# Kernel tuning notes

Hardware: AMD Instinct MI355X
Metric: run time of the kernel (lower is better)

## Reference

```python
import jax, jax.numpy as jnp
import numpy as np

NUM_TYPES = 4
EPS = 1e-5
NEG_SLOPE = 0.01  # nn.LeakyReLU default


def hetero_linear(x, node_type, W, b):
    # x: [N, Cin], W: [T, Cin, Cout], b: [T, Cout]
    # Grouped GEMM via type-masked batched matmul (T is small and fixed).
    onehot = jax.nn.one_hot(node_type, NUM_TYPES, dtype=x.dtype)  # [N, T]
    xt = onehot.T[:, :, None] * x[None, :, :]                      # [T, N, Cin]
    y = jnp.einsum('tni,tio->no', xt, W)                           # [N, Cout]
    return y + b[node_type]


def hetero_batchnorm(x, node_type, gamma, beta):
    # Per-type batch statistics over the nodes of each type (training-mode BN).
    ones = jnp.ones((x.shape[0],), dtype=x.dtype)
    cnt = jax.ops.segment_sum(ones, node_type, num_segments=NUM_TYPES)      # [T]
    cnt = jnp.maximum(cnt, 1.0)
    s = jax.ops.segment_sum(x, node_type, num_segments=NUM_TYPES)           # [T, C]
    ss = jax.ops.segment_sum(x * x, node_type, num_segments=NUM_TYPES)      # [T, C]
    mean = s / cnt[:, None]
    var = ss / cnt[:, None] - mean * mean  # biased variance, as BN uses
    xn = (x - mean[node_type]) * jax.lax.rsqrt(var[node_type] + EPS)
    return xn * gamma[node_type] + beta[node_type]


def setup_inputs() -> dict:
    key = jax.random.key(0)
    ks = jax.random.split(key, 12)
    N, CIN, H, COUT, T = 32768, 256, 512, 256, NUM_TYPES
    x = jax.random.normal(ks[0], (N, CIN), dtype=jnp.float32)
    node_type = jax.random.randint(ks[1], (N,), 0, T, dtype=jnp.int32)
    def lin(k, ci, co):
        k1, k2 = jax.random.split(k)
        scale = 1.0 / np.sqrt(ci)
        W = jax.random.uniform(k1, (T, ci, co), jnp.float32, -scale, scale)
        b = jax.random.uniform(k2, (T, co), jnp.float32, -scale, scale)
        return W, b
    W1, b1 = lin(ks[2], CIN, H)
    W2, b2 = lin(ks[3], H, H)
    W3, b3 = lin(ks[4], H, COUT)
    gamma1 = jnp.ones((T, H), jnp.float32)
    beta1 = jnp.zeros((T, H), jnp.float32)
    gamma2 = jnp.ones((T, H), jnp.float32)
    beta2 = jnp.zeros((T, H), jnp.float32)
    return {"x": x, "node_type": node_type,
            "W1": W1, "b1": b1, "W2": W2, "b2": b2, "W3": W3, "b3": b3,
            "gamma1": gamma1, "beta1": beta1, "gamma2": gamma2, "beta2": beta2}


def reference(x, node_type, W1, b1, W2, b2, W3, b3, gamma1, beta1, gamma2, beta2):
    # Layer 1: HeteroLinear -> HeteroBatchNorm -> LeakyReLU (dropout p=0 -> identity)
    h = hetero_linear(x, node_type, W1, b1)
    h = hetero_batchnorm(h, node_type, gamma1, beta1)
    h = jax.nn.leaky_relu(h, NEG_SLOPE)
    # Layer 2
    h = hetero_linear(h, node_type, W2, b2)
    h = hetero_batchnorm(h, node_type, gamma2, beta2)
    h = jax.nn.leaky_relu(h, NEG_SLOPE)
    # Layer 3: plain_last -> no norm/act
    out = hetero_linear(h, node_type, W3, b3)
    return out
```

## Files before the change

### kernel.cpp

```cpp
#include <hip/hip_runtime.h>
#include <cstdint>
#include <cstddef>

#define N_NODES 32768
#define CIN 256
#define HDIM 512
#define COUT_F 256
#define NTYPE 4
#define ALIGN_SEG 128
#define NPAD (N_NODES + NTYPE * ALIGN_SEG)
#define NROWBLK (NPAD / 128)
#define BN_EPS 1e-5f
#define SLOPE 0.01f

typedef unsigned short u16;
typedef __attribute__((ext_vector_type(8))) short bf16x8;
typedef __attribute__((ext_vector_type(4))) float f32x4;
typedef __attribute__((ext_vector_type(4))) u16 u16x4;

#define GLOBAL_AS __attribute__((address_space(1)))
#define LDS_AS __attribute__((address_space(3)))

__device__ __forceinline__ u16 f2bf(float f) {
  union { float f; unsigned u; } v{f};
  unsigned r = (v.u + 0x7FFF + ((v.u >> 16) & 1)) >> 16;
  return (u16)r;
}
__device__ __forceinline__ float bf2f(u16 b) {
  union { unsigned u; float f; } v;
  v.u = ((unsigned)b) << 16;
  return v.f;
}


__global__ void hist_kernel(const int* __restrict__ nt, int* __restrict__ blockHist) {
  __shared__ int h[NTYPE];
  int tid = threadIdx.x;
  if (tid < NTYPE) h[tid] = 0;
  __syncthreads();
  int i = blockIdx.x * 256 + tid;
  atomicAdd(&h[nt[i]], 1);
  __syncthreads();
  if (tid < NTYPE) blockHist[blockIdx.x * NTYPE + tid] = h[tid];
}

__global__ void scan_kernel(const int* __restrict__ blockHist, int* __restrict__ blockBase,
                            int* __restrict__ meta) {
  int tid = threadIdx.x;
  if (tid < NTYPE) {
    int run = 0;
    for (int b = 0; b < 128; ++b) {
      blockBase[b * NTYPE + tid] = run;
      run += blockHist[b * NTYPE + tid];
    }
    meta[tid] = run;
  }
  __syncthreads();
  if (tid == 0) {
    int s = 0;
    for (int t = 0; t < NTYPE; ++t) {
      meta[4 + t] = s;
      s += (meta[t] + ALIGN_SEG - 1) & ~(ALIGN_SEG - 1);
    }
    meta[8] = s;
  }
}

__global__ void rank_scatter_kernel(const int* __restrict__ nt, const int* __restrict__ blockBase,
                                    const int* __restrict__ meta, int* __restrict__ perm) {
  __shared__ int st[256];
  int tid = threadIdx.x;
  int i = blockIdx.x * 256 + tid;
  int t = nt[i];
  st[tid] = t;
  __syncthreads();
  int rank = 0;
  for (int j = 0; j < tid; ++j) rank += (st[j] == t) ? 1 : 0;
  perm[meta[4 + t] + blockBase[blockIdx.x * NTYPE + t] + rank] = i;
}

__global__ __launch_bounds__(256) void gather_kernel(const float* __restrict__ x,
                                                     const int* __restrict__ perm,
                                                     u16* __restrict__ xs) {
  int p = blockIdx.x * 4 + (threadIdx.x >> 6);
  int lane = threadIdx.x & 63;
  int src = perm[p];
  u16x4* dst = (u16x4*)(xs + (size_t)p * CIN);
  if (src < 0) {
    dst[lane] = (u16x4)0;
  } else {
    float4 v = ((const float4*)(x + (size_t)src * CIN))[lane];
    u16x4 o;
    o.x = f2bf(v.x); o.y = f2bf(v.y); o.z = f2bf(v.z); o.w = f2bf(v.w);
    dst[lane] = o;
  }
}

template <int K, int COUT>
__global__ __launch_bounds__(256) void wtrans_kernel(const float* __restrict__ W,
                                                     u16* __restrict__ Wt) {
  const int t = blockIdx.z;
  const int k0 = blockIdx.x * 32, c0 = blockIdx.y * 32;
  const float* __restrict__ Ws = W + (size_t)t * K * COUT;
  u16* __restrict__ Wd = Wt + (size_t)t * COUT * K;
  __shared__ float tile[32][33];
  int tid = threadIdx.x;
#pragma unroll
  for (int p = 0; p < 4; ++p) {
    int idx = p * 256 + tid;
    int r = idx >> 5, c = idx & 31;
    tile[r][c] = Ws[(size_t)(k0 + r) * COUT + c0 + c];
  }
  __syncthreads();
#pragma unroll
  for (int p = 0; p < 4; ++p) {
    int idx = p * 256 + tid;
    int r = idx >> 5, c = idx & 31;
    Wd[(size_t)(c0 + r) * K + k0 + c] = f2bf(tile[c][r]);
  }
}


template <int K, int COUT, bool SCATTER, bool STATS>
__global__ __launch_bounds__(256, 2) void mfma_gemm_kernel(
    const u16* __restrict__ A, const u16* __restrict__ Wt, const float* __restrict__ bias,
    u16* __restrict__ Yb, float* __restrict__ Yf, float* __restrict__ partS,
    float* __restrict__ partQ, const int* __restrict__ meta, const int* __restrict__ perm) {
  constexpr int GX = COUT / 128;
  const int nwg = (int)(gridDim.x * gridDim.y);
  int l = (int)(blockIdx.y * gridDim.x + blockIdx.x);
  int lid = (l & 7) * (nwg >> 3) + (l >> 3);
  const int bx = lid % GX, by = lid / GX;
  const int col0 = bx * 128, row0 = by * 128;

  const int s1 = meta[5], s2 = meta[6], s3 = meta[7];
  const int t = row0 >= s3 ? 3 : (row0 >= s2 ? 2 : (row0 >= s1 ? 1 : 0));
  const int seg_end = meta[4 + t] + meta[t];
  const u16* __restrict__ Bt = Wt + (size_t)t * COUT * K;

  __shared__ __align__(16) u16 As[2][128 * 64];
  __shared__ __align__(16) u16 Bs[2][128 * 64];

  const int tid = threadIdx.x;
  const int lane = tid & 63;
  const int lr = lane & 15, ls = lane >> 4;
  const int wid = tid >> 6;
  const int wm = wid >> 1, wn = wid & 1;

  int a_off[4][2], b_off[4][2];
#pragma unroll
  for (int i = 0; i < 4; ++i) {
    int r = wm * 64 + i * 16 + lr;
#pragma unroll
    for (int kk = 0; kk < 2; ++kk) a_off[i][kk] = r * 64 + (((kk * 4 + ls)) ^ (r & 7)) * 8;
  }
#pragma unroll
  for (int j = 0; j < 4; ++j) {
    int r = wn * 64 + j * 16 + lr;
#pragma unroll
    for (int kk = 0; kk < 2; ++kk) b_off[j][kk] = r * 64 + (((kk * 4 + ls)) ^ (r & 7)) * 8;
  }

  int st_row[4], st_col[4];
#pragma unroll
  for (int p = 0; p < 4; ++p) {
    int lch = p * 256 + tid;
    int r = lch >> 3, u = lch & 7;
    st_row[p] = r;
    st_col[p] = (u ^ (r & 7)) * 8;
  }
  const int lds_base = (tid & 192) * 8;

  const int nt = K / 64;

  auto stage = [&](int buf, int k0) {
#pragma unroll
    for (int p = 0; p < 4; ++p) {
      const u16* ga = A + (size_t)(row0 + st_row[p]) * K + k0 + st_col[p];
      const u16* gb = Bt + (size_t)(col0 + st_row[p]) * K + k0 + st_col[p];
      __builtin_amdgcn_global_load_lds((const GLOBAL_AS void*)ga,
                                       (LDS_AS void*)(&As[buf][0] + p * 2048 + lds_base), 16, 0, 0);
      __builtin_amdgcn_global_load_lds((const GLOBAL_AS void*)gb,
                                       (LDS_AS void*)(&Bs[buf][0] + p * 2048 + lds_base), 16, 0, 0);
    }
  };

  f32x4 acc[4][4] = {};

  stage(0, 0);
  for (int t8 = 0; t8 < nt; ++t8) {
    const int cur = t8 & 1;
    if (t8 + 1 < nt) {
      stage(cur ^ 1, (t8 + 1) * 64);
      asm volatile("s_waitcnt vmcnt(8)" ::: "memory");
    } else {
      asm volatile("s_waitcnt vmcnt(0)" ::: "memory");
    }
    __builtin_amdgcn_s_barrier();
    __builtin_amdgcn_sched_barrier(0);
#pragma unroll
    for (int kk = 0; kk < 2; ++kk) {
      bf16x8 af[4], bfr[4];
#pragma unroll
      for (int i = 0; i < 4; ++i) af[i] = *(const bf16x8*)(&As[cur][0] + a_off[i][kk]);
#pragma unroll
      for (int j = 0; j < 4; ++j) bfr[j] = *(const bf16x8*)(&Bs[cur][0] + b_off[j][kk]);
#pragma unroll
      for (int i = 0; i < 4; ++i)
#pragma unroll
        for (int j = 0; j < 4; ++j)
          acc[i][j] = __builtin_amdgcn_mfma_f32_16x16x32_bf16(af[i], bfr[j], acc[i][j], 0, 0, 0);
    }
    __builtin_amdgcn_s_barrier();
  }

  float bj[4];
#pragma unroll
  for (int j = 0; j < 4; ++j) bj[j] = bias[(size_t)t * COUT + col0 + wn * 64 + j * 16 + lr];

  if (SCATTER) {
#pragma unroll
    for (int i = 0; i < 4; ++i) {
      int rbase = row0 + wm * 64 + i * 16 + ls * 4;
      int dsts[4];
#pragma unroll
      for (int r = 0; r < 4; ++r) dsts[r] = perm[rbase + r];
#pragma unroll
      for (int j = 0; j < 4; ++j) {
        int gcol = col0 + wn * 64 + j * 16 + lr;
#pragma unroll
        for (int r = 0; r < 4; ++r) {
          if (dsts[r] >= 0) Yf[(size_t)dsts[r] * COUT + gcol] = acc[i][j][r] + bj[j];
        }
      }
    }
  } else {
    float s[4] = {}, q[4] = {};
#pragma unroll
    for (int i = 0; i < 4; ++i) {
      int rbase = row0 + wm * 64 + i * 16 + ls * 4;
#pragma unroll
      for (int j = 0; j < 4; ++j) {
        int gcol = col0 + wn * 64 + j * 16 + lr;
#pragma unroll
        for (int r = 0; r < 4; ++r) {
          int row = rbase + r;
          float y = acc[i][j][r] + bj[j];
          Yb[(size_t)row * COUT + gcol] = f2bf(y);
          if (STATS && row < seg_end) {
            s[j] += y;
            q[j] += y * y;
          }
        }
      }
    }
    if (STATS) {
      float* sred = (float*)&As[0][0];
      float* qred = (float*)&Bs[0][0];
      int slot = (wm * 4 + ls) * 128 + wn * 64 + lr;
      __syncthreads();
#pragma unroll
      for (int j = 0; j < 4; ++j) {
        sred[slot + j * 16] = s[j];
        qred[slot + j * 16] = q[j];
      }
      __syncthreads();
      if (tid < 128) {
        float S = 0.f, Q = 0.f;
#pragma unroll
        for (int k = 0; k < 8; ++k) {
          S += sred[k * 128 + tid];
          Q += qred[k * 128 + tid];
        }
        partS[(size_t)by * COUT + col0 + tid] = S;
        partQ[(size_t)by * COUT + col0 + tid] = Q;
      }
    }
  }
}


__global__ __launch_bounds__(256) void bn_finalize_kernel(const float* __restrict__ partS,
                                                          const float* __restrict__ partQ,
                                                          const int* __restrict__ meta,
                                                          float* __restrict__ mean,
                                                          float* __restrict__ rstd) {
  int idx = blockIdx.x * 256 + threadIdx.x;
  int t = idx >> 9;
  int c = idx & (HDIM - 1);
  int start = meta[4 + t];
  int cnt = meta[t];
  int b0 = start >> 7;
  int nb = (cnt + 127) >> 7;
  float S = 0.f, Q = 0.f;
  for (int b = 0; b < nb; ++b) {
    S += partS[(size_t)(b0 + b) * HDIM + c];
    Q += partQ[(size_t)(b0 + b) * HDIM + c];
  }
  float n = (float)(cnt > 1 ? cnt : 1);
  float m = S / n;
  float var = Q / n - m * m;
  mean[idx] = m;
  rstd[idx] = rsqrtf(fmaxf(var, 0.f) + BN_EPS);
}


__global__ __launch_bounds__(256) void bn_apply_kernel(
    const u16* __restrict__ h, const int* __restrict__ meta, const float* __restrict__ mean,
    const float* __restrict__ rstd, const float* __restrict__ gamma,
    const float* __restrict__ beta, u16* __restrict__ aout) {
  int idx = blockIdx.x * 256 + threadIdx.x;
  int row = idx >> 6;
  int g8 = (idx & 63) * 8;
  const int s1 = meta[5], s2 = meta[6], s3 = meta[7];
  const int t = row >= s3 ? 3 : (row >= s2 ? 2 : (row >= s1 ? 1 : 0));
  size_t base = (size_t)row * HDIM + g8;
  uint4 v = *(const uint4*)(h + base);
  unsigned w[4] = {v.x, v.y, v.z, v.w};
  int tb = t * HDIM + g8;
  float mv[8], rv[8], gv[8], bv[8];
  *(float4*)&mv[0] = *(const float4*)(mean + tb);
  *(float4*)&mv[4] = *(const float4*)(mean + tb + 4);
  *(float4*)&rv[0] = *(const float4*)(rstd + tb);
  *(float4*)&rv[4] = *(const float4*)(rstd + tb + 4);
  *(float4*)&gv[0] = *(const float4*)(gamma + tb);
  *(float4*)&gv[4] = *(const float4*)(gamma + tb + 4);
  *(float4*)&bv[0] = *(const float4*)(beta + tb);
  *(float4*)&bv[4] = *(const float4*)(beta + tb + 4);
  unsigned o[4];
#pragma unroll
  for (int p = 0; p < 4; ++p) {
    u16 lo = (u16)(w[p] & 0xFFFF), hi = (u16)(w[p] >> 16);
    int e0 = p * 2, e1 = p * 2 + 1;
    float sc0 = rv[e0] * gv[e0], sc1 = rv[e1] * gv[e1];
    float y0 = bf2f(lo) * sc0 + (bv[e0] - mv[e0] * sc0);
    float y1 = bf2f(hi) * sc1 + (bv[e1] - mv[e1] * sc1);
    y0 = y0 >= 0.f ? y0 : SLOPE * y0;
    y1 = y1 >= 0.f ? y1 : SLOPE * y1;
    o[p] = (unsigned)f2bf(y0) | ((unsigned)f2bf(y1) << 16);
  }
  *(uint4*)(aout + base) = make_uint4(o[0], o[1], o[2], o[3]);
}


extern "C" void kernel_launch(void* const* d_in, const int* in_sizes, int n_in, void* d_out,
                              int out_size, void* d_ws, size_t ws_size, hipStream_t stream) {
  const float* x = (const float*)d_in[0];
  const int* nt = (const int*)d_in[1];
  const float* W1 = (const float*)d_in[2];
  const float* b1 = (const float*)d_in[3];
  const float* W2 = (const float*)d_in[4];
  const float* b2 = (const float*)d_in[5];
  const float* W3 = (const float*)d_in[6];
  const float* b3 = (const float*)d_in[7];
  const float* g1 = (const float*)d_in[8];
  const float* be1 = (const float*)d_in[9];
  const float* g2 = (const float*)d_in[10];
  const float* be2 = (const float*)d_in[11];
  float* out = (float*)d_out;

  char* ws = (char*)d_ws;
  size_t off = 0;
  auto alloc = [&](size_t bytes) {
    void* p = ws + off;
    off = (off + bytes + 255) & ~(size_t)255;
    return p;
  };
  int* meta = (int*)alloc(16 * 4);
  int* blockHist = (int*)alloc(128 * NTYPE * 4);
  int* blockBase = (int*)alloc(128 * NTYPE * 4);
  int* perm = (int*)alloc((size_t)NPAD * 4);
  float* mean = (float*)alloc((size_t)NTYPE * HDIM * 4);
  float* rstd = (float*)alloc((size_t)NTYPE * HDIM * 4);
  float* partS = (float*)alloc((size_t)NROWBLK * HDIM * 4);
  float* partQ = (float*)alloc((size_t)NROWBLK * HDIM * 4);
  u16* Wt1 = (u16*)alloc((size_t)NTYPE * CIN * HDIM * 2);
  u16* Wt2 = (u16*)alloc((size_t)NTYPE * HDIM * HDIM * 2);
  u16* Wt3 = (u16*)alloc((size_t)NTYPE * HDIM * COUT_F * 2);
  u16* xs = (u16*)alloc((size_t)NPAD * CIN * 2);
  u16* abuf = (u16*)alloc((size_t)NPAD * HDIM * 2);
  u16* hb = (u16*)alloc((size_t)NPAD * HDIM * 2);

  hipMemsetAsync(meta, 0, 64, stream);
  hipMemsetAsync(perm, 0xFF, (size_t)NPAD * 4, stream);
  hist_kernel<<<128, 256, 0, stream>>>(nt, blockHist);
  scan_kernel<<<1, 64, 0, stream>>>(blockHist, blockBase, meta);
  rank_scatter_kernel<<<128, 256, 0, stream>>>(nt, blockBase, meta, perm);
  gather_kernel<<<NPAD / 4, 256, 0, stream>>>(x, perm, xs);

  wtrans_kernel<CIN, HDIM><<<dim3(CIN / 32, HDIM / 32, NTYPE), 256, 0, stream>>>(W1, Wt1);
  wtrans_kernel<HDIM, HDIM><<<dim3(HDIM / 32, HDIM / 32, NTYPE), 256, 0, stream>>>(W2, Wt2);
  wtrans_kernel<HDIM, COUT_F><<<dim3(HDIM / 32, COUT_F / 32, NTYPE), 256, 0, stream>>>(W3, Wt3);

  mfma_gemm_kernel<CIN, HDIM, false, true><<<dim3(HDIM / 128, NPAD / 128), 256, 0, stream>>>(
      xs, Wt1, b1, hb, nullptr, partS, partQ, meta, nullptr);
  bn_finalize_kernel<<<(NTYPE * HDIM) / 256, 256, 0, stream>>>(partS, partQ, meta, mean, rstd);
  bn_apply_kernel<<<(NPAD * (HDIM / 8)) / 256, 256, 0, stream>>>(hb, meta, mean, rstd, g1, be1,
                                                                 abuf);
  mfma_gemm_kernel<HDIM, HDIM, false, true><<<dim3(HDIM / 128, NPAD / 128), 256, 0, stream>>>(
      abuf, Wt2, b2, hb, nullptr, partS, partQ, meta, nullptr);
  bn_finalize_kernel<<<(NTYPE * HDIM) / 256, 256, 0, stream>>>(partS, partQ, meta, mean, rstd);
  bn_apply_kernel<<<(NPAD * (HDIM / 8)) / 256, 256, 0, stream>>>(hb, meta, mean, rstd, g2, be2,
                                                                 abuf);
  mfma_gemm_kernel<HDIM, COUT_F, true, false><<<dim3(COUT_F / 128, NPAD / 128), 256, 0, stream>>>(
      abuf, Wt3, b3, nullptr, out, nullptr, nullptr, meta, perm);
}
```

Baseline: 179.9 us.

## Fuse gather and BN-apply+LeakyReLU into GEMM A-operand loads, enlarge tiles

```diff
diff --git a/kernel.cpp b/kernel.cpp
--- a/kernel.cpp
+++ b/kernel.cpp
@@ -7,9 +7,9 @@
 #define HDIM 512
 #define COUT_F 256
 #define NTYPE 4
-#define ALIGN_SEG 128
+#define ALIGN_SEG 256
 #define NPAD (N_NODES + NTYPE * ALIGN_SEG)
-#define NROWBLK (NPAD / 128)
+#define NROWBLK (NPAD / 256)
 #define BN_EPS 1e-5f
 #define SLOPE 0.01f
 
@@ -18,8 +18,9 @@
 typedef __attribute__((ext_vector_type(4))) float f32x4;
 typedef __attribute__((ext_vector_type(4))) u16 u16x4;
 
-#define GLOBAL_AS __attribute__((address_space(1)))
-#define LDS_AS __attribute__((address_space(3)))
+#define SBAR() __builtin_amdgcn_s_barrier()
+#define SCHED() __builtin_amdgcn_sched_barrier(0)
+#define LGKM0() asm volatile("s_waitcnt lgkmcnt(0)" ::: "memory")
 
 __device__ __forceinline__ u16 f2bf(float f) {
   union { float f; unsigned u; } v{f};
@@ -31,6 +32,7 @@
   v.u = ((unsigned)b) << 16;
   return v.f;
 }
+__device__ __forceinline__ float leaky(float y) { return fmaxf(y, SLOPE * y); }
 
 
 __global__ void hist_kernel(const int* __restrict__ nt, int* __restrict__ blockHist) {
@@ -79,23 +81,6 @@
   perm[meta[4 + t] + blockBase[blockIdx.x * NTYPE + t] + rank] = i;
 }
 
-__global__ __launch_bounds__(256) void gather_kernel(const float* __restrict__ x,
-                                                     const int* __restrict__ perm,
-                                                     u16* __restrict__ xs) {
-  int p = blockIdx.x * 4 + (threadIdx.x >> 6);
-  int lane = threadIdx.x & 63;
-  int src = perm[p];
-  u16x4* dst = (u16x4*)(xs + (size_t)p * CIN);
-  if (src < 0) {
-    dst[lane] = (u16x4)0;
-  } else {
-    float4 v = ((const float4*)(x + (size_t)src * CIN))[lane];
-    u16x4 o;
-    o.x = f2bf(v.x); o.y = f2bf(v.y); o.z = f2bf(v.z); o.w = f2bf(v.w);
-    dst[lane] = o;
-  }
-}
-
 template <int K, int COUT>
 __global__ __launch_bounds__(256) void wtrans_kernel(const float* __restrict__ W,
                                                      u16* __restrict__ Wt) {
@@ -121,25 +106,28 @@
 }
 
 
-template <int K, int COUT, bool SCATTER, bool STATS>
-__global__ __launch_bounds__(256, 2) void mfma_gemm_kernel(
-    const u16* __restrict__ A, const u16* __restrict__ Wt, const float* __restrict__ bias,
+template <int K, int COUT, int MODE, bool SCATTER, bool STATS>
+__global__ __launch_bounds__(512, 2) void mfma_gemm_kernel(
+    const void* __restrict__ Asrc, const int* __restrict__ permIn,
+    const float* __restrict__ scsh, const u16* __restrict__ Wt, const float* __restrict__ bias,
     u16* __restrict__ Yb, float* __restrict__ Yf, float* __restrict__ partS,
-    float* __restrict__ partQ, const int* __restrict__ meta, const int* __restrict__ perm) {
+    float* __restrict__ partQ, const int* __restrict__ meta, const int* __restrict__ permOut) {
   constexpr int GX = COUT / 128;
+  constexpr int ASZ = 256 * 64;
+  constexpr int BSZ = 128 * 64;
   const int nwg = (int)(gridDim.x * gridDim.y);
   int l = (int)(blockIdx.y * gridDim.x + blockIdx.x);
   int lid = (l & 7) * (nwg >> 3) + (l >> 3);
   const int bx = lid % GX, by = lid / GX;
-  const int col0 = bx * 128, row0 = by * 128;
+  const int col0 = bx * 128, row0 = by * 256;
 
   const int s1 = meta[5], s2 = meta[6], s3 = meta[7];
-  const int t = row0 >= s3 ? 3 : (row0 >= s2 ? 2 : (row0 >= s1 ? 1 : 0));
-  const int seg_end = meta[4 + t] + meta[t];
-  const u16* __restrict__ Bt = Wt + (size_t)t * COUT * K;
-
-  __shared__ __align__(16) u16 As[2][128 * 64];
-  __shared__ __align__(16) u16 Bs[2][128 * 64];
+  const int typ = row0 >= s3 ? 3 : (row0 >= s2 ? 2 : (row0 >= s1 ? 1 : 0));
+  const int seg_end = meta[4 + typ] + meta[typ];
+  const u16* __restrict__ Bt = Wt + (size_t)typ * COUT * K;
+
+  __shared__ __align__(16) u16 As[2][ASZ];
+  __shared__ __align__(16) u16 Bs[2][BSZ];
 
   const int tid = threadIdx.x;
   const int lane = tid & 63;
@@ -152,79 +140,146 @@
   for (int i = 0; i < 4; ++i) {
     int r = wm * 64 + i * 16 + lr;
 #pragma unroll
-    for (int kk = 0; kk < 2; ++kk) a_off[i][kk] = r * 64 + (((kk * 4 + ls)) ^ (r & 7)) * 8;
+    for (int kk = 0; kk < 2; ++kk) a_off[i][kk] = r * 64 + ((kk * 4 + ls) ^ (r & 7)) * 8;
   }
 #pragma unroll
   for (int j = 0; j < 4; ++j) {
     int r = wn * 64 + j * 16 + lr;
 #pragma unroll
-    for (int kk = 0; kk < 2; ++kk) b_off[j][kk] = r * 64 + (((kk * 4 + ls)) ^ (r & 7)) * 8;
-  }
-
-  int st_row[4], st_col[4];
-#pragma unroll
-  for (int p = 0; p < 4; ++p) {
-    int lch = p * 256 + tid;
-    int r = lch >> 3, u = lch & 7;
-    st_row[p] = r;
-    st_col[p] = (u ^ (r & 7)) * 8;
-  }
-  const int lds_base = (tid & 192) * 8;
-
-  const int nt = K / 64;
-
-  auto stage = [&](int buf, int k0) {
-#pragma unroll
-    for (int p = 0; p < 4; ++p) {
-      const u16* ga = A + (size_t)(row0 + st_row[p]) * K + k0 + st_col[p];
-      const u16* gb = Bt + (size_t)(col0 + st_row[p]) * K + k0 + st_col[p];
-      __builtin_amdgcn_global_load_lds((const GLOBAL_AS void*)ga,
-                                       (LDS_AS void*)(&As[buf][0] + p * 2048 + lds_base), 16, 0, 0);
-      __builtin_amdgcn_global_load_lds((const GLOBAL_AS void*)gb,
-                                       (LDS_AS void*)(&Bs[buf][0] + p * 2048 + lds_base), 16, 0, 0);
-    }
+    for (int kk = 0; kk < 2; ++kk) b_off[j][kk] = r * 64 + ((kk * 4 + ls) ^ (r & 7)) * 8;
+  }
+
+  const int cOct = tid & 7;
+  const int rbase = tid >> 3;
+  const int xr = (cOct ^ (rbase & 7)) * 8;
+  int wrA[4], wrB[2];
+#pragma unroll
+  for (int p = 0; p < 4; ++p) wrA[p] = (p * 64 + rbase) * 64 + xr;
+#pragma unroll
+  for (int p = 0; p < 2; ++p) wrB[p] = (p * 64 + rbase) * 64 + xr;
+
+  int srcRow[4];
+  if (MODE == 0) {
+#pragma unroll
+    for (int p = 0; p < 4; ++p) srcRow[p] = permIn[row0 + p * 64 + rbase];
+  }
+
+  const int nsteps = K / 64;
+
+  uint4 aD[4];
+  float4 fD[4][2];
+  float4 sV[4];
+  uint4 bD[2];
+
+  auto loads = [&](int k0) {
+    if (MODE == 0) {
+      const float* X = (const float*)Asrc;
+#pragma unroll
+      for (int p = 0; p < 4; ++p) {
+        int sp = srcRow[p];
+        const float4* xp = (const float4*)(X + (size_t)(sp < 0 ? 0 : sp) * CIN + k0 + cOct * 8);
+        fD[p][0] = xp[0];
+        fD[p][1] = xp[1];
+        if (sp < 0) {
+          fD[p][0] = make_float4(0.f, 0.f, 0.f, 0.f);
+          fD[p][1] = make_float4(0.f, 0.f, 0.f, 0.f);
+        }
+      }
+    } else {
+      const u16* Ab = (const u16*)Asrc;
+#pragma unroll
+      for (int p = 0; p < 4; ++p)
+        aD[p] = *(const uint4*)(Ab + (size_t)(row0 + p * 64 + rbase) * K + k0 + cOct * 8);
+      const float4* sp = (const float4*)(scsh + ((size_t)typ * HDIM + k0 + cOct * 8) * 2);
+#pragma unroll
+      for (int e = 0; e < 4; ++e) sV[e] = sp[e];
+    }
+#pragma unroll
+    for (int p = 0; p < 2; ++p)
+      bD[p] = *(const uint4*)(Bt + (size_t)(col0 + p * 64 + rbase) * K + k0 + cOct * 8);
   };
 
+  auto applyWrite = [&](int buf) {
+    u16* ab = &As[0][0] + buf * ASZ;
+    u16* bb = &Bs[0][0] + buf * BSZ;
+    if (MODE == 0) {
+#pragma unroll
+      for (int p = 0; p < 4; ++p) {
+        uint4 o;
+        o.x = (unsigned)f2bf(fD[p][0].x) | ((unsigned)f2bf(fD[p][0].y) << 16);
+        o.y = (unsigned)f2bf(fD[p][0].z) | ((unsigned)f2bf(fD[p][0].w) << 16);
+        o.z = (unsigned)f2bf(fD[p][1].x) | ((unsigned)f2bf(fD[p][1].y) << 16);
+        o.w = (unsigned)f2bf(fD[p][1].z) | ((unsigned)f2bf(fD[p][1].w) << 16);
+        *(uint4*)(ab + wrA[p]) = o;
+      }
+    } else {
+#pragma unroll
+      for (int p = 0; p < 4; ++p) {
+        unsigned w[4] = {aD[p].x, aD[p].y, aD[p].z, aD[p].w};
+        uint4 o;
+        unsigned oo[4];
+#pragma unroll
+        for (int e2 = 0; e2 < 4; ++e2) {
+          float z0 = bf2f((u16)(w[e2] & 0xFFFF));
+          float z1 = bf2f((u16)(w[e2] >> 16));
+          float y0 = leaky(z0 * sV[e2].x + sV[e2].y);
+          float y1 = leaky(z1 * sV[e2].z + sV[e2].w);
+          oo[e2] = (unsigned)f2bf(y0) | ((unsigned)f2bf(y1) << 16);
+        }
+        o.x = oo[0]; o.y = oo[1]; o.z = oo[2]; o.w = oo[3];
+        *(uint4*)(ab + wrA[p]) = o;
+      }
+    }
+#pragma unroll
+    for (int p = 0; p < 2; ++p) *(uint4*)(bb + wrB[p]) = bD[p];
+  };
+
   f32x4 acc[4][4] = {};
 
-  stage(0, 0);
-  for (int t8 = 0; t8 < nt; ++t8) {
+  loads(0);
+  applyWrite(0);
+  loads(64);
+  LGKM0();
+  SBAR();
+  SCHED();
+
+  for (int t8 = 0; t8 < nsteps; ++t8) {
     const int cur = t8 & 1;
-    if (t8 + 1 < nt) {
-      stage(cur ^ 1, (t8 + 1) * 64);
-      asm volatile("s_waitcnt vmcnt(8)" ::: "memory");
-    } else {
-      asm volatile("s_waitcnt vmcnt(0)" ::: "memory");
-    }
-    __builtin_amdgcn_s_barrier();
-    __builtin_amdgcn_sched_barrier(0);
+    if (t8 + 1 < nsteps) {
+      applyWrite(cur ^ 1);
+      if (t8 + 2 < nsteps) loads((t8 + 2) * 64);
+    }
+    const u16* Ab = &As[0][0] + cur * ASZ;
+    const u16* Bb = &Bs[0][0] + cur * BSZ;
 #pragma unroll
     for (int kk = 0; kk < 2; ++kk) {
       bf16x8 af[4], bfr[4];
 #pragma unroll
-      for (int i = 0; i < 4; ++i) af[i] = *(const bf16x8*)(&As[cur][0] + a_off[i][kk]);
-#pragma unroll
-      for (int j = 0; j < 4; ++j) bfr[j] = *(const bf16x8*)(&Bs[cur][0] + b_off[j][kk]);
+      for (int i = 0; i < 4; ++i) af[i] = *(const bf16x8*)(Ab + a_off[i][kk]);
+#pragma unroll
+      for (int j = 0; j < 4; ++j) bfr[j] = *(const bf16x8*)(Bb + b_off[j][kk]);
 #pragma unroll
       for (int i = 0; i < 4; ++i)
 #pragma unroll
         for (int j = 0; j < 4; ++j)
           acc[i][j] = __builtin_amdgcn_mfma_f32_16x16x32_bf16(af[i], bfr[j], acc[i][j], 0, 0, 0);
     }
-    __builtin_amdgcn_s_barrier();
+    LGKM0();
+    SBAR();
+    SCHED();
   }
 
   float bj[4];
 #pragma unroll
-  for (int j = 0; j < 4; ++j) bj[j] = bias[(size_t)t * COUT + col0 + wn * 64 + j * 16 + lr];
+  for (int j = 0; j < 4; ++j) bj[j] = bias[(size_t)typ * COUT + col0 + wn * 64 + j * 16 + lr];
 
   if (SCATTER) {
 #pragma unroll
     for (int i = 0; i < 4; ++i) {
-      int rbase = row0 + wm * 64 + i * 16 + ls * 4;
+      int rbase2 = row0 + wm * 64 + i * 16 + ls * 4;
       int dsts[4];
 #pragma unroll
-      for (int r = 0; r < 4; ++r) dsts[r] = perm[rbase + r];
+      for (int r = 0; r < 4; ++r) dsts[r] = permOut[rbase2 + r];
 #pragma unroll
       for (int j = 0; j < 4; ++j) {
         int gcol = col0 + wn * 64 + j * 16 + lr;
@@ -238,13 +293,13 @@
     float s[4] = {}, q[4] = {};
 #pragma unroll
     for (int i = 0; i < 4; ++i) {
-      int rbase = row0 + wm * 64 + i * 16 + ls * 4;
+      int rbase2 = row0 + wm * 64 + i * 16 + ls * 4;
 #pragma unroll
       for (int j = 0; j < 4; ++j) {
         int gcol = col0 + wn * 64 + j * 16 + lr;
 #pragma unroll
         for (int r = 0; r < 4; ++r) {
-          int row = rbase + r;
+          int row = rbase2 + r;
           float y = acc[i][j][r] + bj[j];
           Yb[(size_t)row * COUT + gcol] = f2bf(y);
           if (STATS && row < seg_end) {
@@ -257,18 +312,19 @@
     if (STATS) {
       float* sred = (float*)&As[0][0];
       float* qred = (float*)&Bs[0][0];
-      int slot = (wm * 4 + ls) * 128 + wn * 64 + lr;
+      int grp = wm * 4 + ls;
       __syncthreads();
 #pragma unroll
       for (int j = 0; j < 4; ++j) {
-        sred[slot + j * 16] = s[j];
-        qred[slot + j * 16] = q[j];
+        int colIdx = wn * 64 + j * 16 + lr;
+        sred[grp * 128 + colIdx] = s[j];
+        qred[grp * 128 + colIdx] = q[j];
       }
       __syncthreads();
       if (tid < 128) {
         float S = 0.f, Q = 0.f;
 #pragma unroll
-        for (int k = 0; k < 8; ++k) {
+        for (int k = 0; k < 16; ++k) {
           S += sred[k * 128 + tid];
           Q += qred[k * 128 + tid];
         }
@@ -283,15 +339,16 @@
 __global__ __launch_bounds__(256) void bn_finalize_kernel(const float* __restrict__ partS,
                                                           const float* __restrict__ partQ,
                                                           const int* __restrict__ meta,
-                                                          float* __restrict__ mean,
-                                                          float* __restrict__ rstd) {
+                                                          const float* __restrict__ gamma,
+                                                          const float* __restrict__ beta,
+                                                          float* __restrict__ scsh) {
   int idx = blockIdx.x * 256 + threadIdx.x;
   int t = idx >> 9;
   int c = idx & (HDIM - 1);
   int start = meta[4 + t];
   int cnt = meta[t];
-  int b0 = start >> 7;
-  int nb = (cnt + 127) >> 7;
+  int b0 = start >> 8;
+  int nb = (cnt + 255) >> 8;
   float S = 0.f, Q = 0.f;
   for (int b = 0; b < nb; ++b) {
     S += partS[(size_t)(b0 + b) * HDIM + c];
@@ -300,46 +357,11 @@
   float n = (float)(cnt > 1 ? cnt : 1);
   float m = S / n;
   float var = Q / n - m * m;
-  mean[idx] = m;
-  rstd[idx] = rsqrtf(fmaxf(var, 0.f) + BN_EPS);
-}
-
-
-__global__ __launch_bounds__(256) void bn_apply_kernel(
-    const u16* __restrict__ h, const int* __restrict__ meta, const float* __restrict__ mean,
-    const float* __restrict__ rstd, const float* __restrict__ gamma,
-    const float* __restrict__ beta, u16* __restrict__ aout) {
-  int idx = blockIdx.x * 256 + threadIdx.x;
-  int row = idx >> 6;
-  int g8 = (idx & 63) * 8;
-  const int s1 = meta[5], s2 = meta[6], s3 = meta[7];
-  const int t = row >= s3 ? 3 : (row >= s2 ? 2 : (row >= s1 ? 1 : 0));
-  size_t base = (size_t)row * HDIM + g8;
-  uint4 v = *(const uint4*)(h + base);
-  unsigned w[4] = {v.x, v.y, v.z, v.w};
-  int tb = t * HDIM + g8;
-  float mv[8], rv[8], gv[8], bv[8];
-  *(float4*)&mv[0] = *(const float4*)(mean + tb);
-  *(float4*)&mv[4] = *(const float4*)(mean + tb + 4);
-  *(float4*)&rv[0] = *(const float4*)(rstd + tb);
-  *(float4*)&rv[4] = *(const float4*)(rstd + tb + 4);
-  *(float4*)&gv[0] = *(const float4*)(gamma + tb);
-  *(float4*)&gv[4] = *(const float4*)(gamma + tb + 4);
-  *(float4*)&bv[0] = *(const float4*)(beta + tb);
-  *(float4*)&bv[4] = *(const float4*)(beta + tb + 4);
-  unsigned o[4];
-#pragma unroll
-  for (int p = 0; p < 4; ++p) {
-    u16 lo = (u16)(w[p] & 0xFFFF), hi = (u16)(w[p] >> 16);
-    int e0 = p * 2, e1 = p * 2 + 1;
-    float sc0 = rv[e0] * gv[e0], sc1 = rv[e1] * gv[e1];
-    float y0 = bf2f(lo) * sc0 + (bv[e0] - mv[e0] * sc0);
-    float y1 = bf2f(hi) * sc1 + (bv[e1] - mv[e1] * sc1);
-    y0 = y0 >= 0.f ? y0 : SLOPE * y0;
-    y1 = y1 >= 0.f ? y1 : SLOPE * y1;
-    o[p] = (unsigned)f2bf(y0) | ((unsigned)f2bf(y1) << 16);
-  }
-  *(uint4*)(aout + base) = make_uint4(o[0], o[1], o[2], o[3]);
+  float rs = rsqrtf(fmaxf(var, 0.f) + BN_EPS);
+  float sc = rs * gamma[idx];
+  float sh = beta[idx] - m * sc;
+  scsh[(size_t)idx * 2] = sc;
+  scsh[(size_t)idx * 2 + 1] = sh;
 }
 
 
@@ -370,38 +392,35 @@
   int* blockHist = (int*)alloc(128 * NTYPE * 4);
   int* blockBase = (int*)alloc(128 * NTYPE * 4);
   int* perm = (int*)alloc((size_t)NPAD * 4);
-  float* mean = (float*)alloc((size_t)NTYPE * HDIM * 4);
-  float* rstd = (float*)alloc((size_t)NTYPE * HDIM * 4);
+  float* scsh1 = (float*)alloc((size_t)NTYPE * HDIM * 2 * 4);
+  float* scsh2 = (float*)alloc((size_t)NTYPE * HDIM * 2 * 4);
   float* partS = (float*)alloc((size_t)NROWBLK * HDIM * 4);
   float* partQ = (float*)alloc((size_t)NROWBLK * HDIM * 4);
   u16* Wt1 = (u16*)alloc((size_t)NTYPE * CIN * HDIM * 2);
   u16* Wt2 = (u16*)alloc((size_t)NTYPE * HDIM * HDIM * 2);
   u16* Wt3 = (u16*)alloc((size_t)NTYPE * HDIM * COUT_F * 2);
-  u16* xs = (u16*)alloc((size_t)NPAD * CIN * 2);
-  u16* abuf = (u16*)alloc((size_t)NPAD * HDIM * 2);
-  u16* hb = (u16*)alloc((size_t)NPAD * HDIM * 2);
+  u16* hb1 = (u16*)alloc((size_t)NPAD * HDIM * 2);
+  u16* hb2 = (u16*)alloc((size_t)NPAD * HDIM * 2);
 
   hipMemsetAsync(meta, 0, 64, stream);
   hipMemsetAsync(perm, 0xFF, (size_t)NPAD * 4, stream);
   hist_kernel<<<128, 256, 0, stream>>>(nt, blockHist);
   scan_kernel<<<1, 64, 0, stream>>>(blockHist, blockBase, meta);
   rank_scatter_kernel<<<128, 256, 0, stream>>>(nt, blockBase, meta, perm);
-  gather_kernel<<<NPAD / 4, 256, 0, stream>>>(x, perm, xs);
 
   wtrans_kernel<CIN, HDIM><<<dim3(CIN / 32, HDIM / 32, NTYPE), 256, 0, stream>>>(W1, Wt1);
   wtrans_kernel<HDIM, HDIM><<<dim3(HDIM / 32, HDIM / 32, NTYPE), 256, 0, stream>>>(W2, Wt2);
   wtrans_kernel<HDIM, COUT_F><<<dim3(HDIM / 32, COUT_F / 32, NTYPE), 256, 0, stream>>>(W3, Wt3);
 
-  mfma_gemm_kernel<CIN, HDIM, false, true><<<dim3(HDIM / 128, NPAD / 128), 256, 0, stream>>>(
-      xs, Wt1, b1, hb, nullptr, partS, partQ, meta, nullptr);
-  bn_finalize_kernel<<<(NTYPE * HDIM) / 256, 256, 0, stream>>>(partS, partQ, meta, mean, rstd);
-  bn_apply_kernel<<<(NPAD * (HDIM / 8)) / 256, 256, 0, stream>>>(hb, meta, mean, rstd, g1, be1,
-                                                                 abuf);
-  mfma_gemm_kernel<HDIM, HDIM, false, true><<<dim3(HDIM / 128, NPAD / 128), 256, 0, stream>>>(
-      abuf, Wt2, b2, hb, nullptr, partS, partQ, meta, nullptr);
-  bn_finalize_kernel<<<(NTYPE * HDIM) / 256, 256, 0, stream>>>(partS, partQ, meta, mean, rstd);
-  bn_apply_kernel<<<(NPAD * (HDIM / 8)) / 256, 256, 0, stream>>>(hb, meta, mean, rstd, g2, be2,
-                                                                 abuf);
-  mfma_gemm_kernel<HDIM, COUT_F, true, false><<<dim3(COUT_F / 128, NPAD / 128), 256, 0, stream>>>(
-      abuf, Wt3, b3, nullptr, out, nullptr, nullptr, meta, perm);
-}
+  mfma_gemm_kernel<CIN, HDIM, 0, false, true>
+      <<<dim3(HDIM / 128, NPAD / 256), 512, 0, stream>>>(x, perm, nullptr, Wt1, b1, hb1, nullptr,
+                                                         partS, partQ, meta, nullptr);
+  bn_finalize_kernel<<<(NTYPE * HDIM) / 256, 256, 0, stream>>>(partS, partQ, meta, g1, be1, scsh1);
+  mfma_gemm_kernel<HDIM, HDIM, 1, false, true>
+      <<<dim3(HDIM / 128, NPAD / 256), 512, 0, stream>>>(hb1, nullptr, scsh1, Wt2, b2, hb2,
+                                                         nullptr, partS, partQ, meta, nullptr);
+  bn_finalize_kernel<<<(NTYPE * HDIM) / 256, 256, 0, stream>>>(partS, partQ, meta, g2, be2, scsh2);
+  mfma_gemm_kernel<HDIM, COUT_F, 1, true, false>
+      <<<dim3(COUT_F / 128, NPAD / 256), 512, 0, stream>>>(hb2, nullptr, scsh2, Wt3, b3, nullptr,
+                                                           out, nullptr, nullptr, meta, perm);
+}
```

New measurement: 201.5 us. 12.0% more time.

## Switch GEMM to 256x128 tiles with 512 threads and K-step 32

Applied to the files above, without the earlier changes.

```diff
diff --git a/kernel.cpp b/kernel.cpp
--- a/kernel.cpp
+++ b/kernel.cpp
@@ -7,9 +7,9 @@
 #define HDIM 512
 #define COUT_F 256
 #define NTYPE 4
-#define ALIGN_SEG 128
+#define ALIGN_SEG 256
 #define NPAD (N_NODES + NTYPE * ALIGN_SEG)
-#define NROWBLK (NPAD / 128)
+#define NROWBLK (NPAD / 256)
 #define BN_EPS 1e-5f
 #define SLOPE 0.01f
 
@@ -20,6 +20,8 @@
 
 #define GLOBAL_AS __attribute__((address_space(1)))
 #define LDS_AS __attribute__((address_space(3)))
+#define SBAR() __builtin_amdgcn_s_barrier()
+#define SCHED() __builtin_amdgcn_sched_barrier(0)
 
 __device__ __forceinline__ u16 f2bf(float f) {
   union { float f; unsigned u; } v{f};
@@ -122,24 +124,26 @@
 
 
 template <int K, int COUT, bool SCATTER, bool STATS>
-__global__ __launch_bounds__(256, 2) void mfma_gemm_kernel(
+__global__ __launch_bounds__(512, 4) void mfma_gemm_kernel(
     const u16* __restrict__ A, const u16* __restrict__ Wt, const float* __restrict__ bias,
     u16* __restrict__ Yb, float* __restrict__ Yf, float* __restrict__ partS,
     float* __restrict__ partQ, const int* __restrict__ meta, const int* __restrict__ perm) {
   constexpr int GX = COUT / 128;
+  constexpr int ASZ = 256 * 32;
+  constexpr int BSZ = 128 * 32;
   const int nwg = (int)(gridDim.x * gridDim.y);
   int l = (int)(blockIdx.y * gridDim.x + blockIdx.x);
   int lid = (l & 7) * (nwg >> 3) + (l >> 3);
   const int bx = lid % GX, by = lid / GX;
-  const int col0 = bx * 128, row0 = by * 128;
+  const int col0 = bx * 128, row0 = by * 256;
 
   const int s1 = meta[5], s2 = meta[6], s3 = meta[7];
   const int t = row0 >= s3 ? 3 : (row0 >= s2 ? 2 : (row0 >= s1 ? 1 : 0));
   const int seg_end = meta[4 + t] + meta[t];
   const u16* __restrict__ Bt = Wt + (size_t)t * COUT * K;
 
-  __shared__ __align__(16) u16 As[2][128 * 64];
-  __shared__ __align__(16) u16 Bs[2][128 * 64];
+  __shared__ __align__(16) u16 As[2][ASZ];
+  __shared__ __align__(16) u16 Bs[2][BSZ];
 
   const int tid = threadIdx.x;
   const int lane = tid & 63;
@@ -147,71 +151,69 @@
   const int wid = tid >> 6;
   const int wm = wid >> 1, wn = wid & 1;
 
-  int a_off[4][2], b_off[4][2];
+  int a_off[4], b_off[4];
 #pragma unroll
   for (int i = 0; i < 4; ++i) {
     int r = wm * 64 + i * 16 + lr;
-#pragma unroll
-    for (int kk = 0; kk < 2; ++kk) a_off[i][kk] = r * 64 + (((kk * 4 + ls)) ^ (r & 7)) * 8;
+    a_off[i] = r * 32 + (ls ^ ((r >> 1) & 3)) * 8;
   }
 #pragma unroll
   for (int j = 0; j < 4; ++j) {
     int r = wn * 64 + j * 16 + lr;
-#pragma unroll
-    for (int kk = 0; kk < 2; ++kk) b_off[j][kk] = r * 64 + (((kk * 4 + ls)) ^ (r & 7)) * 8;
-  }
-
-  int st_row[4], st_col[4];
-#pragma unroll
-  for (int p = 0; p < 4; ++p) {
-    int lch = p * 256 + tid;
-    int r = lch >> 3, u = lch & 7;
-    st_row[p] = r;
-    st_col[p] = (u ^ (r & 7)) * 8;
-  }
-  const int lds_base = (tid & 192) * 8;
-
-  const int nt = K / 64;
+    b_off[j] = r * 32 + (ls ^ ((r >> 1) & 3)) * 8;
+  }
+
+  int stA_row[2], stA_col[2];
+#pragma unroll
+  for (int p = 0; p < 2; ++p) {
+    int lch = p * 512 + tid;
+    int r = lch >> 2;
+    stA_row[p] = r;
+    stA_col[p] = ((lch & 3) ^ ((r >> 1) & 3)) * 8;
+  }
+  const int stB_row = tid >> 2;
+  const int stB_col = ((tid & 3) ^ ((stB_row >> 1) & 3)) * 8;
+  const int ldsW = (tid & 448) * 8;
+
+  const int nsteps = K / 32;
 
   auto stage = [&](int buf, int k0) {
 #pragma unroll
-    for (int p = 0; p < 4; ++p) {
-      const u16* ga = A + (size_t)(row0 + st_row[p]) * K + k0 + st_col[p];
-      const u16* gb = Bt + (size_t)(col0 + st_row[p]) * K + k0 + st_col[p];
+    for (int p = 0; p < 2; ++p) {
+      const u16* ga = A + (size_t)(row0 + stA_row[p]) * K + k0 + stA_col[p];
       __builtin_amdgcn_global_load_lds((const GLOBAL_AS void*)ga,
-                                       (LDS_AS void*)(&As[buf][0] + p * 2048 + lds_base), 16, 0, 0);
-      __builtin_amdgcn_global_load_lds((const GLOBAL_AS void*)gb,
-                                       (LDS_AS void*)(&Bs[buf][0] + p * 2048 + lds_base), 16, 0, 0);
-    }
+                                       (LDS_AS void*)(&As[buf][0] + p * 4096 + ldsW), 16, 0, 0);
+    }
+    const u16* gb = Bt + (size_t)(col0 + stB_row) * K + k0 + stB_col;
+    __builtin_amdgcn_global_load_lds((const GLOBAL_AS void*)gb,
+                                     (LDS_AS void*)(&Bs[buf][0] + ldsW), 16, 0, 0);
   };
 
   f32x4 acc[4][4] = {};
 
   stage(0, 0);
-  for (int t8 = 0; t8 < nt; ++t8) {
+  for (int t8 = 0; t8 < nsteps; ++t8) {
     const int cur = t8 & 1;
-    if (t8 + 1 < nt) {
-      stage(cur ^ 1, (t8 + 1) * 64);
-      asm volatile("s_waitcnt vmcnt(8)" ::: "memory");
+    if (t8 + 1 < nsteps) {
+      stage(cur ^ 1, (t8 + 1) * 32);
+      asm volatile("s_waitcnt vmcnt(3)" ::: "memory");
     } else {
       asm volatile("s_waitcnt vmcnt(0)" ::: "memory");
     }
-    __builtin_amdgcn_s_barrier();
-    __builtin_amdgcn_sched_barrier(0);
-#pragma unroll
-    for (int kk = 0; kk < 2; ++kk) {
-      bf16x8 af[4], bfr[4];
-#pragma unroll
-      for (int i = 0; i < 4; ++i) af[i] = *(const bf16x8*)(&As[cur][0] + a_off[i][kk]);
-#pragma unroll
-      for (int j = 0; j < 4; ++j) bfr[j] = *(const bf16x8*)(&Bs[cur][0] + b_off[j][kk]);
-#pragma unroll
-      for (int i = 0; i < 4; ++i)
-#pragma unroll
-        for (int j = 0; j < 4; ++j)
-          acc[i][j] = __builtin_amdgcn_mfma_f32_16x16x32_bf16(af[i], bfr[j], acc[i][j], 0, 0, 0);
-    }
-    __builtin_amdgcn_s_barrier();
+    SBAR();
+    SCHED();
+    bf16x8 af[4], bfr[4];
+#pragma unroll
+    for (int i = 0; i < 4; ++i) af[i] = *(const bf16x8*)(&As[cur][0] + a_off[i]);
+#pragma unroll
+    for (int j = 0; j < 4; ++j) bfr[j] = *(const bf16x8*)(&Bs[cur][0] + b_off[j]);
+#pragma unroll
+    for (int i = 0; i < 4; ++i)
+#pragma unroll
+      for (int j = 0; j < 4; ++j)
+        acc[i][j] = __builtin_amdgcn_mfma_f32_16x16x32_bf16(af[i], bfr[j], acc[i][j], 0, 0, 0);
+    SBAR();
+    SCHED();
   }
 
   float bj[4];
@@ -257,18 +259,19 @@
     if (STATS) {
       float* sred = (float*)&As[0][0];
       float* qred = (float*)&Bs[0][0];
-      int slot = (wm * 4 + ls) * 128 + wn * 64 + lr;
+      int grp = wm * 4 + ls;
       __syncthreads();
 #pragma unroll
       for (int j = 0; j < 4; ++j) {
-        sred[slot + j * 16] = s[j];
-        qred[slot + j * 16] = q[j];
+        int colIdx = wn * 64 + j * 16 + lr;
+        sred[grp * 128 + colIdx] = s[j];
+        qred[grp * 128 + colIdx] = q[j];
       }
       __syncthreads();
       if (tid < 128) {
         float S = 0.f, Q = 0.f;
 #pragma unroll
-        for (int k = 0; k < 8; ++k) {
+        for (int k = 0; k < 16; ++k) {
           S += sred[k * 128 + tid];
           Q += qred[k * 128 + tid];
         }
@@ -290,8 +293,8 @@
   int c = idx & (HDIM - 1);
   int start = meta[4 + t];
   int cnt = meta[t];
-  int b0 = start >> 7;
-  int nb = (cnt + 127) >> 7;
+  int b0 = start >> 8;
+  int nb = (cnt + 255) >> 8;
   float S = 0.f, Q = 0.f;
   for (int b = 0; b < nb; ++b) {
     S += partS[(size_t)(b0 + b) * HDIM + c];
@@ -392,16 +395,19 @@
   wtrans_kernel<HDIM, HDIM><<<dim3(HDIM / 32, HDIM / 32, NTYPE), 256, 0, stream>>>(W2, Wt2);
   wtrans_kernel<HDIM, COUT_F><<<dim3(HDIM / 32, COUT_F / 32, NTYPE), 256, 0, stream>>>(W3, Wt3);
 
-  mfma_gemm_kernel<CIN, HDIM, false, true><<<dim3(HDIM / 128, NPAD / 128), 256, 0, stream>>>(
-      xs, Wt1, b1, hb, nullptr, partS, partQ, meta, nullptr);
+  mfma_gemm_kernel<CIN, HDIM, false, true>
+      <<<dim3(HDIM / 128, NPAD / 256), 512, 0, stream>>>(xs, Wt1, b1, hb, nullptr, partS, partQ,
+                                                         meta, nullptr);
   bn_finalize_kernel<<<(NTYPE * HDIM) / 256, 256, 0, stream>>>(partS, partQ, meta, mean, rstd);
   bn_apply_kernel<<<(NPAD * (HDIM / 8)) / 256, 256, 0, stream>>>(hb, meta, mean, rstd, g1, be1,
                                                                  abuf);
-  mfma_gemm_kernel<HDIM, HDIM, false, true><<<dim3(HDIM / 128, NPAD / 128), 256, 0, stream>>>(
-      abuf, Wt2, b2, hb, nullptr, partS, partQ, meta, nullptr);
+  mfma_gemm_kernel<HDIM, HDIM, false, true>
+      <<<dim3(HDIM / 128, NPAD / 256), 512, 0, stream>>>(abuf, Wt2, b2, hb, nullptr, partS, partQ,
+                                                         meta, nullptr);
   bn_finalize_kernel<<<(NTYPE * HDIM) / 256, 256, 0, stream>>>(partS, partQ, meta, mean, rstd);
   bn_apply_kernel<<<(NPAD * (HDIM / 8)) / 256, 256, 0, stream>>>(hb, meta, mean, rstd, g2, be2,
                                                                  abuf);
-  mfma_gemm_kernel<HDIM, COUT_F, true, false><<<dim3(COUT_F / 128, NPAD / 128), 256, 0, stream>>>(
-      abuf, Wt3, b3, nullptr, out, nullptr, nullptr, meta, perm);
-}
+  mfma_gemm_kernel<HDIM, COUT_F, true, false>
+      <<<dim3(COUT_F / 128, NPAD / 256), 512, 0, stream>>>(abuf, Wt3, b3, nullptr, out, nullptr,
+                                                           nullptr, meta, perm);
+}
```

Result: faster. 166.3 us (-7.5%).
